# Performance work log

Measured on AMD Instinct MI355X. Metric: run time of the kernel, lower is better.

The kernel has to match this reference:

```python
import jax, jax.numpy as jnp
import numpy as np

NEIGHBOR_NUM = 16
POOLING_RATE = 4


def setup_inputs() -> dict:
    key = jax.random.key(0)
    k1, k2, k3 = jax.random.split(key, 3)
    bs, v, c = 16, 2048, 512
    vertices = jax.random.normal(k1, (bs, v, 3), dtype=jnp.float32)
    feature_map = jax.random.normal(k2, (bs, v, c), dtype=jnp.float32)
    pool_num = v // POOLING_RATE  # 512
    sample_idx = jax.random.randint(k3, (pool_num,), 0, v, dtype=jnp.int32)
    return {"vertices": vertices, "feature_map": feature_map, "sample_idx": sample_idx}


def _get_neighbor_index(vertices, neighbor_num):
    # vertices: (bs, v, 3) -> (bs, v, neighbor_num)
    inner = jnp.einsum("bnd,bmd->bnm", vertices, vertices)  # (bs, v, v)
    quadratic = jnp.sum(vertices * vertices, axis=2)  # (bs, v)
    distance = -2.0 * inner + quadratic[:, None, :] + quadratic[:, :, None]
    k = min(neighbor_num + 1, vertices.shape[1])
    # smallest-k == top-k of negated distance; drop self (first column)
    _, idx = jax.lax.top_k(-distance, k)  # (bs, v, k)
    return idx[:, :, 1:]


def reference(vertices, feature_map, sample_idx):
    neighbor_index = _get_neighbor_index(vertices, NEIGHBOR_NUM)  # (bs, v, n)
    # gather per-batch: (bs, v, n, c)
    neighbor_feature = jax.vmap(lambda f, i: f[i])(feature_map, neighbor_index)
    pooled_feature = jnp.max(neighbor_feature, axis=2)  # (bs, v, c)
    vertices_pool = vertices[:, sample_idx, :]  # (bs, pool_num, 3)
    feature_map_pool = pooled_feature[:, sample_idx, :]  # (bs, pool_num, c)
    return (vertices_pool, feature_map_pool)
```

## Files before the change

### kernel.cpp

```cpp
#include <hip/hip_runtime.h>

#define BS 16
#define V  2048
#define C  512
#define PN 512
#define K  16
#define NT 256

typedef unsigned long long u64;
typedef unsigned int u32;

template<int CTRL>
__device__ __forceinline__ u32 min_dpp_u32(u32 x) {
    const u32 n = (u32)__builtin_amdgcn_update_dpp((int)x, (int)x, CTRL, 0xF, 0xF, false);
    return n < x ? n : x;
}
__device__ __forceinline__ u32 wave_min_u32(u32 x) {
    x = min_dpp_u32<0x111>(x);
    x = min_dpp_u32<0x112>(x);
    x = min_dpp_u32<0x114>(x);
    x = min_dpp_u32<0x118>(x);
    x = min_dpp_u32<0x142>(x);
    x = min_dpp_u32<0x143>(x);
    return (u32)__builtin_amdgcn_readlane((int)x, 63);
}
template<int CTRL>
__device__ __forceinline__ u64 max_dpp_u64(u64 x) {
    const int lo = (int)(u32)x, hi = (int)(u32)(x >> 32);
    const int plo = __builtin_amdgcn_update_dpp(lo, lo, CTRL, 0xF, 0xF, false);
    const int phi = __builtin_amdgcn_update_dpp(hi, hi, CTRL, 0xF, 0xF, false);
    const u64 p = ((u64)(u32)phi << 32) | (u32)plo;
    return p > x ? p : x;
}
template<int OFS>
__device__ __forceinline__ u64 swz_u64(u64 x) {
    const int lo = __builtin_amdgcn_ds_swizzle((int)(u32)x, OFS);
    const int hi = __builtin_amdgcn_ds_swizzle((int)(u32)(x >> 32), OFS);
    return ((u64)(u32)hi << 32) | (u32)lo;
}
template<int D, int OFS>
__device__ __forceinline__ u64 bitonic_stage(u64 x, int ll) {
    const u64 p = swz_u64<OFS>(x);
    const bool keepmin = ((ll & D) == 0);
    const bool pl = (p < x);
    const bool takep = keepmin ? pl : !pl;
    return takep ? p : x;
}
__device__ __forceinline__ int mbcnt64(u64 m) {
    return __builtin_amdgcn_mbcnt_hi((u32)(m >> 32),
           __builtin_amdgcn_mbcnt_lo((u32)m, 0));
}

#define CE(i, j) { const bool p_ = sk[j] < sk[i]; const u64 a_ = p_ ? sk[j] : sk[i]; \
                   const u64 b_ = p_ ? sk[i] : sk[j]; sk[i] = a_; sk[j] = b_; }

#define POP_ONE(SLOT)                                                          \
    {                                                                          \
        const u32 wm = wave_min_u32(d0);                                       \
        const bool pred = (d0 == wm);                                          \
        const u64 mask = __ballot(pred);                                       \
        const int cnt = (int)__popcll(mask);                                   \
        const u64 hid = __ballot(d1 == wm);                                    \
        bool w_;                                                               \
        if ((cnt == 1) && (hid == 0ull)) {                                     \
            w_ = pred;                                                         \
        } else {                                                               \
            const u32 myidx = pred ? (wbase + ((perm & 15u) << 6) + (u32)lane) \
                                   : 0xFFFFFFFFu;                              \
            const u32 wi = wave_min_u32(myidx);                                \
            w_ = pred && (myidx == wi);                                        \
        }                                                                      \
        if (w_) {                                                              \
            const u32 idx = wbase + ((perm & 15u) << 6) + (u32)lane;           \
            wlist[wid * 16 + (SLOT)] = ((u64)d0 << 32) | idx;                  \
        }                                                                      \
        d0 = w_ ? d1 : d0; d1 = w_ ? d2 : d1; d2 = w_ ? d3 : d2;               \
        d3 = w_ ? d4 : d3; d4 = w_ ? d5 : d4; d5 = w_ ? d6 : d5;               \
        d6 = w_ ? d7 : d6; d7 = w_ ? 0xFFFFFFFFu : d7;                         \
        perm = w_ ? (perm >> 4) : perm;                                        \
    }

__global__ __launch_bounds__(NT) void pool_knn_kernel(
    const float* __restrict__ vert,
    const float* __restrict__ feat,
    const int*   __restrict__ sidx,
    float* __restrict__ out)
{
    const int blk = blockIdx.x;
    const int b = blk >> 9;
    const int s = blk & (PN - 1);
    const int t = threadIdx.x;
    const int wid = t >> 6;
    const int lane = t & 63;
    const u32 wbase = (u32)wid * 512u;

    __shared__ u64 wlist[64];
    __shared__ int nbr[K];
    __shared__ int flagw;
    __shared__ int cntw[4];
    if (t == 0) flagw = 0;
    if (t < 4) cntw[t] = 8;

    const int q = sidx[s];
    const float* vb = vert + (size_t)b * (V * 3);
    const float qx = vb[q * 3 + 0];
    const float qy = vb[q * 3 + 1];
    const float qz = vb[q * 3 + 2];
    const float qq = qx * qx + qy * qy + qz * qz;

    u32 d0, d1, d2, d3, d4, d5, d6, d7, perm;
    {
        u64 sk[8];
        #pragma unroll
        for (int i = 0; i < 8; ++i) {
            const int m = (int)wbase + i * 64 + lane;
            const float mx = vb[m * 3 + 0];
            const float my = vb[m * 3 + 1];
            const float mz = vb[m * 3 + 2];
            const float qm = mx * mx + my * my + mz * mz;
            const float inner = qx * mx + qy * my + qz * mz;
            const float dist = (-2.0f * inner + qm) + qq;
            u32 u = __float_as_uint(dist);
            u ^= (u & 0x80000000u) ? 0xFFFFFFFFu : 0x80000000u;
            if (m == q) u = 0xFFFFFFFFu;
            sk[i] = ((u64)u << 32) | (u32)i;
        }
        CE(0,1) CE(2,3) CE(4,5) CE(6,7)
        CE(0,2) CE(1,3) CE(4,6) CE(5,7)
        CE(1,2) CE(5,6) CE(0,4) CE(3,7)
        CE(1,5) CE(2,6)
        CE(1,4) CE(3,6)
        CE(2,4) CE(3,5)
        CE(3,4)
        d0 = (u32)(sk[0] >> 32); d1 = (u32)(sk[1] >> 32);
        d2 = (u32)(sk[2] >> 32); d3 = (u32)(sk[3] >> 32);
        d4 = (u32)(sk[4] >> 32); d5 = (u32)(sk[5] >> 32);
        d6 = (u32)(sk[6] >> 32); d7 = (u32)(sk[7] >> 32);
        perm = (u32)sk[0]        | ((u32)sk[1] << 4)  | ((u32)sk[2] << 8)  |
               ((u32)sk[3] << 12)| ((u32)sk[4] << 16) | ((u32)sk[5] << 20) |
               ((u32)sk[6] << 24)| ((u32)sk[7] << 28);
    }

    #pragma unroll
    for (int r = 0; r < 8; ++r) { POP_ONE(r) }
    __syncthreads();

    u64 x;
    {
        const int w = lane >> 3;
        const int rr = (w & 1) ? (7 - (lane & 7)) : (lane & 7);
        const int addr = (w & 3) * 16 + rr;
        const u64 ld = wlist[(lane < 32) ? addr : 0];
        x = (lane < 32) ? ld : ~0ULL;
        const int ll = lane & 15;
        x = bitonic_stage<8, 0x201F>(x, ll);
        x = bitonic_stage<4, 0x101F>(x, ll);
        x = bitonic_stage<2, 0x081F>(x, ll);
        x = bitonic_stage<1, 0x041F>(x, ll);
        const u64 p = swz_u64<0x7C1F>(x);
        x = (p < x) ? p : x;
    }

    u64 B16;
    {
        u64 bm = (lane < 16) ? x : 0ULL;
        bm = max_dpp_u64<0x121>(bm);
        bm = max_dpp_u64<0x122>(bm);
        bm = max_dpp_u64<0x124>(bm);
        bm = max_dpp_u64<0x128>(bm);
        const u32 blo = (u32)__builtin_amdgcn_readlane((int)(u32)bm, 0);
        const u32 bhi = (u32)__builtin_amdgcn_readlane((int)(u32)(bm >> 32), 0);
        B16 = ((u64)bhi << 32) | blo;
    }
    const u64 k8 = wlist[wid * 16 + 7];
    const int resu = __builtin_amdgcn_readfirstlane((int)(k8 < B16));
    if (resu && lane == 0) flagw = 1;
    __syncthreads();

    int nidx[K];
    if (flagw != 0) {
        if (resu) {
            int r = 8;
            while (r < 16) {
                const u32 fm = wave_min_u32(d0);
                if (((u64)fm << 32) > B16) break;
                POP_ONE(r)
                ++r;
            }
            if (lane == 0) cntw[wid] = r;
        }
        __syncthreads();
        if (wid == 0) {
            const int cv = cntw[lane >> 4];
            const u64 ck = ((lane & 15) < cv) ? wlist[lane] : ~0ULL;
            u32 cd = (u32)(ck >> 32);
            const u32 ci = (u32)ck;
            int r = 0;
            while (r < K) {
                const u32 wm = wave_min_u32(cd);
                const bool pred = (cd == wm);
                const u64 mask = __ballot(pred);
                const int cnt = (int)__popcll(mask);
                if (r + cnt <= K) {
                    if (pred) nbr[r + mbcnt64(mask)] = (int)ci;
                    cd = pred ? 0xFFFFFFFFu : cd;
                    r += cnt;
                } else {
                    const u32 mi = pred ? ci : 0xFFFFFFFFu;
                    const u32 wi = wave_min_u32(mi);
                    const bool w2 = pred && (ci == wi);
                    if (w2) nbr[r] = (int)ci;
                    cd = w2 ? 0xFFFFFFFFu : cd;
                    r += 1;
                }
            }
        }
        __syncthreads();
        #pragma unroll
        for (int r = 0; r < K; ++r)
            nidx[r] = __builtin_amdgcn_readfirstlane(nbr[r]);
    } else {
        const int xlo = (int)(u32)x;
        #pragma unroll
        for (int r = 0; r < K; ++r)
            nidx[r] = __builtin_amdgcn_readlane(xlo, r);
    }

    const float* fb = feat + (size_t)b * (V * C);
    const int ch = t * 2;
    float m0 = -__builtin_inff(), m1 = -__builtin_inff();
    #pragma unroll
    for (int r = 0; r < K; ++r) {
        const float2 f = *reinterpret_cast<const float2*>(fb + (size_t)nidx[r] * C + ch);
        m0 = fmaxf(m0, f.x);
        m1 = fmaxf(m1, f.y);
    }
    float* o1 = out + (size_t)BS * PN * 3 + (size_t)(b * PN + s) * C + ch;
    o1[0] = m0;
    o1[1] = m1;

    if (t < 3) {
        out[(size_t)(b * PN + s) * 3 + t] = vb[q * 3 + t];
    }
}

extern "C" void kernel_launch(void* const* d_in, const int* in_sizes, int n_in,
                              void* d_out, int out_size, void* d_ws, size_t ws_size,
                              hipStream_t stream) {
    const float* vert = (const float*)d_in[0];
    const float* feat = (const float*)d_in[1];
    const int*   sidx = (const int*)d_in[2];
    float* out = (float*)d_out;

    pool_knn_kernel<<<BS * PN, NT, 0, stream>>>(vert, feat, sidx, out);
}
```

Baseline: 129.8 us.

## Move merge to wave 0, swizzle block-to-batch mapping, simplify tie check

```diff
diff --git a/kernel.cpp b/kernel.cpp
--- a/kernel.cpp
+++ b/kernel.cpp
@@ -59,10 +59,8 @@
         const u32 wm = wave_min_u32(d0);                                       \
         const bool pred = (d0 == wm);                                          \
         const u64 mask = __ballot(pred);                                       \
-        const int cnt = (int)__popcll(mask);                                   \
-        const u64 hid = __ballot(d1 == wm);                                    \
         bool w_;                                                               \
-        if ((cnt == 1) && (hid == 0ull)) {                                     \
+        if (__popcll(mask) == 1) {                                             \
             w_ = pred;                                                         \
         } else {                                                               \
             const u32 myidx = pred ? (wbase + ((perm & 15u) << 6) + (u32)lane) \
@@ -86,19 +84,19 @@
     const int*   __restrict__ sidx,
     float* __restrict__ out)
 {
-    const int blk = blockIdx.x;
-    const int b = blk >> 9;
-    const int s = blk & (PN - 1);
+    const int wk = ((blockIdx.x & 7) << 10) | (blockIdx.x >> 3);
+    const int b = wk >> 9;
+    const int s = wk & (PN - 1);
     const int t = threadIdx.x;
     const int wid = t >> 6;
     const int lane = t & 63;
     const u32 wbase = (u32)wid * 512u;
 
     __shared__ u64 wlist[64];
+    __shared__ u64 sB16;
     __shared__ int nbr[K];
     __shared__ int flagw;
     __shared__ int cntw[4];
-    if (t == 0) flagw = 0;
     if (t < 4) cntw[t] = 8;
 
     const int q = sidx[s];
@@ -145,45 +143,49 @@
     for (int r = 0; r < 8; ++r) { POP_ONE(r) }
     __syncthreads();
 
-    u64 x;
-    {
-        const int w = lane >> 3;
-        const int rr = (w & 1) ? (7 - (lane & 7)) : (lane & 7);
-        const int addr = (w & 3) * 16 + rr;
-        const u64 ld = wlist[(lane < 32) ? addr : 0];
-        x = (lane < 32) ? ld : ~0ULL;
-        const int ll = lane & 15;
-        x = bitonic_stage<8, 0x201F>(x, ll);
-        x = bitonic_stage<4, 0x101F>(x, ll);
-        x = bitonic_stage<2, 0x081F>(x, ll);
-        x = bitonic_stage<1, 0x041F>(x, ll);
-        const u64 p = swz_u64<0x7C1F>(x);
-        x = (p < x) ? p : x;
-    }
-
-    u64 B16;
-    {
-        u64 bm = (lane < 16) ? x : 0ULL;
-        bm = max_dpp_u64<0x121>(bm);
-        bm = max_dpp_u64<0x122>(bm);
-        bm = max_dpp_u64<0x124>(bm);
-        bm = max_dpp_u64<0x128>(bm);
-        const u32 blo = (u32)__builtin_amdgcn_readlane((int)(u32)bm, 0);
-        const u32 bhi = (u32)__builtin_amdgcn_readlane((int)(u32)(bm >> 32), 0);
-        B16 = ((u64)bhi << 32) | blo;
-    }
-    const u64 k8 = wlist[wid * 16 + 7];
-    const int resu = __builtin_amdgcn_readfirstlane((int)(k8 < B16));
-    if (resu && lane == 0) flagw = 1;
+    if (wid == 0) {
+        u64 x;
+        {
+            const int w = lane >> 3;
+            const int rr = (w & 1) ? (7 - (lane & 7)) : (lane & 7);
+            const int addr = (w & 3) * 16 + rr;
+            const u64 ld = wlist[(lane < 32) ? addr : 0];
+            x = (lane < 32) ? ld : ~0ULL;
+            const int ll = lane & 15;
+            x = bitonic_stage<8, 0x201F>(x, ll);
+            x = bitonic_stage<4, 0x101F>(x, ll);
+            x = bitonic_stage<2, 0x081F>(x, ll);
+            x = bitonic_stage<1, 0x041F>(x, ll);
+            const u64 p = swz_u64<0x7C1F>(x);
+            x = (p < x) ? p : x;
+        }
+        if (lane < 16) nbr[lane] = (int)(u32)x;
+        u64 B16;
+        {
+            u64 bm = (lane < 16) ? x : 0ULL;
+            bm = max_dpp_u64<0x121>(bm);
+            bm = max_dpp_u64<0x122>(bm);
+            bm = max_dpp_u64<0x124>(bm);
+            bm = max_dpp_u64<0x128>(bm);
+            const u32 blo = (u32)__builtin_amdgcn_readlane((int)(u32)bm, 0);
+            const u32 bhi = (u32)__builtin_amdgcn_readlane((int)(u32)(bm >> 32), 0);
+            B16 = ((u64)bhi << 32) | blo;
+        }
+        const u64 k8w = wlist[(lane & 3) * 16 + 7];
+        const bool rp = (lane < 4) && (k8w < B16);
+        const int resmask = (int)(__ballot(rp) & 0xFull);
+        if (lane == 0) { flagw = resmask; sB16 = B16; }
+    }
     __syncthreads();
 
-    int nidx[K];
-    if (flagw != 0) {
-        if (resu) {
+    const int fl = flagw;
+    if (fl != 0) {
+        const u64 B16v = sB16;
+        if ((fl >> wid) & 1) {
             int r = 8;
             while (r < 16) {
                 const u32 fm = wave_min_u32(d0);
-                if (((u64)fm << 32) > B16) break;
+                if (((u64)fm << 32) > B16v) break;
                 POP_ONE(r)
                 ++r;
             }
@@ -216,15 +218,12 @@
             }
         }
         __syncthreads();
-        #pragma unroll
-        for (int r = 0; r < K; ++r)
-            nidx[r] = __builtin_amdgcn_readfirstlane(nbr[r]);
-    } else {
-        const int xlo = (int)(u32)x;
-        #pragma unroll
-        for (int r = 0; r < K; ++r)
-            nidx[r] = __builtin_amdgcn_readlane(xlo, r);
-    }
+    }
+
+    int nidx[K];
+    #pragma unroll
+    for (int r = 0; r < K; ++r)
+        nidx[r] = __builtin_amdgcn_readfirstlane(nbr[r]);
 
     const float* fb = feat + (size_t)b * (V * C);
     const int ch = t * 2;
```

Result: slower. 132.8 us (+2.3%).
